# Kernel optimization log

Hardware: AMD Instinct MI355X
Metric: run time of the kernel (lower is better)

## Reference

```python
import jax, jax.numpy as jnp
import numpy as np

B = 64       # number of graphs
R = 148      # fixed ROI count from source
D = 64       # hidden_channels (embed_dim, 4 heads)
H = 4
IN1 = 64     # node feature dim (after stripping label column)
INR = 148    # roi-graph feature dim
HID = 1000
NCLS = 2
N1 = 262144
E1 = 1048576
N2 = B * R
E2 = 262144
EPS = 1e-5


def setup_inputs() -> dict:
    key = jax.random.key(0)
    ks = jax.random.split(key, 40)
    def p(i, shape, s=0.1):
        return jax.random.normal(ks[i], shape, dtype=jnp.float32) * s
    inp = {
        'x_feat': jax.random.normal(ks[0], (N1, IN1), dtype=jnp.float32),
        'node_roi': jax.random.randint(ks[1], (N1,), 0, R, dtype=jnp.int32),
        'batch1': ((jnp.arange(N1, dtype=jnp.int32) * B) // N1).astype(jnp.int32),
        'edge_index1': jax.random.randint(ks[2], (2, E1), 0, N1, dtype=jnp.int32),
        'edge_weight1': jax.random.uniform(ks[3], (E1,), dtype=jnp.float32, minval=0.1, maxval=1.0),
        'x2_feat': jax.random.normal(ks[4], (N2, INR), dtype=jnp.float32),
        'roi_labels2': (jnp.arange(N2, dtype=jnp.int32) % R).astype(jnp.int32),
        'batch2': (jnp.arange(N2, dtype=jnp.int32) // R).astype(jnp.int32),
        'edge_index2': jax.random.randint(ks[5], (2, E2), 0, N2, dtype=jnp.int32),
        'edge_weight2': jax.random.uniform(ks[6], (E2,), dtype=jnp.float32, minval=0.1, maxval=1.0),
        'Wg1': p(7, (IN1, D)), 'bg1': jnp.zeros((D,), jnp.float32),
        'Wg2': p(8, (D, D)), 'bg2': jnp.zeros((D,), jnp.float32),
        'Wr1': p(9, (INR, D)), 'br1': jnp.zeros((D,), jnp.float32),
        'Wr2': p(10, (D, D)), 'br2': jnp.zeros((D,), jnp.float32),
        'in_proj_w': p(11, (3 * D, D)), 'in_proj_b': jnp.zeros((3 * D,), jnp.float32),
        'out_proj_w': p(12, (D, D)), 'out_proj_b': jnp.zeros((D,), jnp.float32),
        'ln1_g': jnp.ones((D,), jnp.float32), 'ln1_b': jnp.zeros((D,), jnp.float32),
        'ff_w1': p(13, (D, D)), 'ff_b1': jnp.zeros((D,), jnp.float32),
        'ff_w2': p(14, (D, D)), 'ff_b2': jnp.zeros((D,), jnp.float32),
        'ln2_g': jnp.ones((D,), jnp.float32), 'ln2_b': jnp.zeros((D,), jnp.float32),
        'Wc1': p(15, (R * D, HID), 0.02), 'bc1': jnp.zeros((HID,), jnp.float32),
        'bn_g': jnp.ones((HID,), jnp.float32), 'bn_b': jnp.zeros((HID,), jnp.float32),
        'Wc2': p(16, (HID, NCLS), 0.02), 'bc2': jnp.zeros((NCLS,), jnp.float32),
    }
    return inp


def gcn_conv(h, src, dst, ew, W, b, n):
    # PyG GCNConv w/ edge weights: add self-loops (weight 1), sym-normalize.
    h = h @ W
    deg = jax.ops.segment_sum(ew, dst, num_segments=n) + 1.0
    dinv = jax.lax.rsqrt(deg)
    norm = dinv[src] * ew * dinv[dst]                      # (E,)
    agg = jax.ops.segment_sum(h[src] * norm[:, None], dst, num_segments=n)
    agg = agg + h * (dinv * dinv)[:, None]                 # self-loop term
    return agg + b


def roi_pool_mean(h, roi, batch):
    # fused scatter mean keyed by (batch, roi) -> (B, R, d); empty slots stay 0
    seg = batch * R + roi
    sums = jax.ops.segment_sum(h, seg, num_segments=B * R)
    cnt = jax.ops.segment_sum(jnp.ones_like(h[:, 0]), seg, num_segments=B * R)
    return (sums / jnp.maximum(cnt, 1.0)[:, None]).reshape(B, R, h.shape[1])


def layer_norm(x, g, b):
    mu = x.mean(axis=-1, keepdims=True)
    var = x.var(axis=-1, keepdims=True)
    return (x - mu) * jax.lax.rsqrt(var + EPS) * g + b


def reference(x_feat, node_roi, batch1, edge_index1, edge_weight1,
              x2_feat, roi_labels2, batch2, edge_index2, edge_weight2,
              Wg1, bg1, Wg2, bg2, Wr1, br1, Wr2, br2,
              in_proj_w, in_proj_b, out_proj_w, out_proj_b,
              ln1_g, ln1_b, ff_w1, ff_b1, ff_w2, ff_b2, ln2_g, ln2_b,
              Wc1, bc1, bn_g, bn_b, Wc2, bc2):
    s1, d1 = edge_index1[0], edge_index1[1]
    s2, d2 = edge_index2[0], edge_index2[1]

    # ROI-graph branch (convs_roi[:-1]): 2 GCN layers, relu, eval dropout=noop
    h2 = jax.nn.relu(gcn_conv(x2_feat, s2, d2, edge_weight2, Wr1, br1, N2))
    h2 = jax.nn.relu(gcn_conv(h2, s2, d2, edge_weight2, Wr2, br2, N2))
    pooled_roi = roi_pool_mean(h2, roi_labels2, batch2)          # (B,R,D)

    # node-graph branch (convs[:-1])
    h1 = jax.nn.relu(gcn_conv(x_feat, s1, d1, edge_weight1, Wg1, bg1, N1))
    h1 = jax.nn.relu(gcn_conv(h1, s1, d1, edge_weight1, Wg2, bg2, N1))
    pooled = roi_pool_mean(h1, node_roi, batch1)                 # (B,R,D)

    combined = pooled + pooled_roi                               # transformer_in_combined

    # SelfAttnBlock (torch MultiheadAttention, batch_first, 4 heads)
    hd = D // H
    qkv = combined @ in_proj_w.T + in_proj_b                     # (B,R,3D)
    q, k, v = jnp.split(qkv, 3, axis=-1)
    q = q.reshape(B, R, H, hd)
    k = k.reshape(B, R, H, hd)
    v = v.reshape(B, R, H, hd)
    scores = jnp.einsum('bqhd,bkhd->bhqk', q, k) / np.sqrt(hd).astype(np.float32)
    attn_w = jax.nn.softmax(scores, axis=-1)                     # (B,H,R,R)
    o = jnp.einsum('bhqk,bkhd->bqhd', attn_w, v).reshape(B, R, D)
    o = o @ out_proj_w.T + out_proj_b
    x = layer_norm(combined + o, ln1_g, ln1_b)
    f = jax.nn.relu(x @ ff_w1 + ff_b1) @ ff_w2 + ff_b2
    t_out = layer_norm(x + f, ln2_g, ln2_b)                      # (B,R,D)

    # classifier: Linear -> BatchNorm1d(eval: mean0,var1) -> LeakyReLU -> Linear
    z = t_out.reshape(B, R * D) @ Wc1 + bc1
    z = bn_g * z * jax.lax.rsqrt(jnp.asarray(1.0 + EPS, z.dtype)) + bn_b
    z = jnp.where(z >= 0, z, 0.01 * z)
    out = z @ Wc2 + bc2                                          # (B,NCLS)
    return (out, pooled, pooled_roi, t_out, attn_w)
```

## Files before the change

kernel.cpp:

```cpp
#include <hip/hip_runtime.h>
#include <cstdint>
#include <cstddef>

#define N1v 262144
#define E1v 1048576
#define N2v 9472
#define E2v 262144
#define BBv 64
#define RRv 148
#define HIDv 1000
#define BRv (BBv * RRv)
#define NSEG 9472
#define EPB 4096
#define NBK1 256
#define SH1 10
#define BINS1 1024
#define CAP1 4864
#define NBK2 74
#define SH2 7
#define BINS2 128
#define CAP2 4096

__host__ __device__ constexpr int cdiv(int a, int b) { return (a + b - 1) / b; }

typedef __attribute__((ext_vector_type(8))) short bf16x8;
typedef __attribute__((ext_vector_type(4))) float f32x4;
typedef unsigned short ushort_t;
typedef unsigned long long u64;

__device__ inline short f2bf(float f) {
    union { float f; unsigned u; } v; v.f = f;
    unsigned r = v.u + 0x7fff + ((v.u >> 16) & 1);
    return (short)(r >> 16);
}
__device__ inline float bf2f(unsigned hs) {
    union { unsigned u; float f; } v; v.u = hs << 16; return v.f;
}
__device__ inline unsigned relu_pk(unsigned u) {
    unsigned r = u;
    if (r & 0x8000u) r &= 0xFFFF0000u;
    if (r & 0x80000000u) r &= 0x0000FFFFu;
    return r;
}

__global__ __launch_bounds__(256) void k_binA(const int* __restrict__ dst1, int* __restrict__ bc1,
                                              const int* __restrict__ dst2, int* __restrict__ bc2) {
    int bid = blockIdx.x;
    const int* dst; int* bc; int nbk, sh, e0;
    if (bid < E1v / EPB) { dst = dst1; bc = bc1; nbk = NBK1; sh = SH1; e0 = bid * EPB; }
    else { dst = dst2; bc = bc2; nbk = NBK2; sh = SH2; e0 = (bid - E1v / EPB) * EPB; }
    __shared__ int h[256];
    int tid = threadIdx.x;
    if (tid < nbk) h[tid] = 0;
    __syncthreads();
    for (int t = tid; t < EPB; t += 256) atomicAdd(&h[dst[e0 + t] >> sh], 1);
    __syncthreads();
    if (tid < nbk && h[tid]) atomicAdd(&bc[tid], h[tid]);
}

__global__ __launch_bounds__(256) void k_scanAB(const int* __restrict__ bc1, int* __restrict__ bb1, int* __restrict__ cur1,
                                                const int* __restrict__ bc2, int* __restrict__ bb2, int* __restrict__ cur2) {
    __shared__ int tmp[256];
    int t = threadIdx.x;
    int v = bc1[t];
    tmp[t] = v; __syncthreads();
    int val = v;
    for (int off = 1; off < 256; off <<= 1) { int o = (t >= off) ? tmp[t - off] : 0; __syncthreads(); val += o; tmp[t] = val; __syncthreads(); }
    int excl = val - v;
    bb1[t] = excl; cur1[t] = excl;
    if (t == 255) bb1[256] = val;
    __syncthreads();
    int v2 = (t < NBK2) ? bc2[t] : 0;
    tmp[t] = v2; __syncthreads();
    int val2 = v2;
    for (int off = 1; off < 256; off <<= 1) { int o = (t >= off) ? tmp[t - off] : 0; __syncthreads(); val2 += o; tmp[t] = val2; __syncthreads(); }
    if (t < NBK2) { int e2 = val2 - v2; bb2[t] = e2; cur2[t] = e2; }
    if (t == NBK2 - 1) bb2[NBK2] = val2;
}

__global__ __launch_bounds__(256) void k_binB(const int* __restrict__ src1, const int* __restrict__ dst1,
                                              const float* __restrict__ ew1, int* __restrict__ cur1, u64* __restrict__ rb1,
                                              const int* __restrict__ src2, const int* __restrict__ dst2,
                                              const float* __restrict__ ew2, int* __restrict__ cur2, u64* __restrict__ rb2) {
    int bid = blockIdx.x;
    const int* src; const int* dst; const float* ew; int* cur; u64* rb; int nbk, sh, e0;
    if (bid < E1v / EPB) { src = src1; dst = dst1; ew = ew1; cur = cur1; rb = rb1; nbk = NBK1; sh = SH1; e0 = bid * EPB; }
    else { src = src2; dst = dst2; ew = ew2; cur = cur2; rb = rb2; nbk = NBK2; sh = SH2; e0 = (bid - E1v / EPB) * EPB; }
    __shared__ int h[256], basg[256];
    int tid = threadIdx.x;
    if (tid < nbk) h[tid] = 0;
    __syncthreads();
    for (int t = tid; t < EPB; t += 256) atomicAdd(&h[dst[e0 + t] >> sh], 1);
    __syncthreads();
    if (tid < nbk) {
        int c = h[tid];
        basg[tid] = c ? atomicAdd(&cur[tid], c) : 0;
        h[tid] = 0;
    }
    __syncthreads();
    unsigned lowmask = (1u << sh) - 1u;
    for (int t = tid; t < EPB; t += 256) {
        int d = dst[e0 + t];
        int b = d >> sh;
        int r = atomicAdd(&h[b], 1);
        unsigned lo = ((unsigned)src[e0 + t] << sh) | ((unsigned)d & lowmask);
        rb[(size_t)basg[b] + r] = ((u64)(unsigned)__float_as_int(ew[e0 + t]) << 32) | lo;
    }
}

template<int BINS, int CAP, int SH>
__global__ __launch_bounds__(256) void k_csrC(const u64* __restrict__ rb, const int* __restrict__ bb,
                                              float* __restrict__ dinv, int* __restrict__ offs,
                                              int2* __restrict__ snC) {
    int b = blockIdx.x;
    int beg = bb[b], end = bb[b + 1], cnt = end - beg;
    __shared__ int hist[BINS];
    __shared__ float degs[BINS];
    __shared__ int scn[BINS];
    __shared__ int tmp[256];
    extern __shared__ int2 outb[];
    int tid = threadIdx.x;
    for (int i = tid; i < BINS; i += 256) { hist[i] = 0; degs[i] = 0.f; }
    __syncthreads();
    for (int j = beg + tid; j < end; j += 256) {
        u64 rec = rb[j];
        int bin = (int)((unsigned)rec & (BINS - 1));
        float w = __int_as_float((int)(rec >> 32));
        atomicAdd(&hist[bin], 1);
        atomicAdd(&degs[bin], w);
    }
    __syncthreads();
    constexpr int PER = (BINS + 255) / 256;
    int lv[PER];
    int tsum = 0;
    int base_i = tid * PER;
#pragma unroll
    for (int k = 0; k < PER; ++k) { int idx = base_i + k; lv[k] = (idx < BINS) ? hist[idx] : 0; tsum += lv[k]; }
    tmp[tid] = tsum; __syncthreads();
    int val = tsum;
    for (int off = 1; off < 256; off <<= 1) { int o = (tid >= off) ? tmp[tid - off] : 0; __syncthreads(); val += o; tmp[tid] = val; __syncthreads(); }
    int run = val - tsum;
#pragma unroll
    for (int k = 0; k < PER; ++k) { int idx = base_i + k; if (idx < BINS) { scn[idx] = run; run += lv[k]; } }
    __syncthreads();
    for (int i = tid; i < BINS; i += 256) {
        offs[b * BINS + i] = beg + scn[i];
        dinv[b * BINS + i] = rsqrtf(degs[i] + 1.0f);
    }
    __syncthreads();
    bool staged = (cnt <= CAP);
    for (int j = beg + tid; j < end; j += 256) {
        u64 rec = rb[j];
        unsigned lo = (unsigned)rec;
        int bin = (int)(lo & (BINS - 1));
        int s = (int)(lo >> SH);
        int wbits = (int)(rec >> 32);
        int r = atomicAdd(&scn[bin], 1);
        int2 o2 = make_int2(s, wbits);
        if (staged) outb[r] = o2;
        else snC[(size_t)beg + r] = o2;
    }
    __syncthreads();
    if (staged) {
        for (int j = tid; j < cnt; j += 256) snC[(size_t)beg + j] = outb[j];
    }
}

__global__ __launch_bounds__(256) void k_pool_csr(const int* __restrict__ roi, int* __restrict__ offs_p,
                                                  int* __restrict__ nodeC) {
    int b = blockIdx.x;
    __shared__ int rl[4096];
    __shared__ int hist[RRv];
    __shared__ int curs[RRv];
    int tid = threadIdx.x;
    for (int t = tid; t < RRv; t += 256) hist[t] = 0;
    __syncthreads();
    int base = b * 4096;
    for (int t = tid; t < 4096; t += 256) {
        int r = roi[base + t];
        rl[t] = r;
        atomicAdd(&hist[r], 1);
    }
    __syncthreads();
    if (tid < RRv) {
        int s = 0;
        for (int k = 0; k < tid; ++k) s += hist[k];
        curs[tid] = s;
        offs_p[b * RRv + tid] = base + s;
    }
    __syncthreads();
    for (int t = tid; t < 4096; t += 256) {
        int r = rl[t];
        int j = atomicAdd(&curs[r], 1);
        nodeC[base + j] = base + t;
    }
}

__global__ __launch_bounds__(256) void k_pool_gather(const int* __restrict__ nodeC, const int* __restrict__ offs,
                                                     const ushort_t* __restrict__ Ab, float* __restrict__ pooled) {
    int tid = threadIdx.x;
    int lane = tid & 63;
    int es = lane >> 4;
    int fq = lane & 15;
    int gw = blockIdx.x * 4 + (tid >> 6);
    int tw = gridDim.x * 4;
    for (int s = gw; s < NSEG; s += tw) {
        int beg = offs[s];
        int end = (s + 1 < NSEG) ? offs[s + 1] : N1v;
        float ax = 0.f, ay = 0.f, az = 0.f, aw = 0.f;
        for (int j = beg + es; j < end; j += 4) {
            int node = nodeC[j];
            uint2 v = *(const uint2*)(Ab + (size_t)node * 64 + fq * 4);
            ax += fmaxf(bf2f(v.x & 0xffffu), 0.f);
            ay += fmaxf(bf2f(v.x >> 16), 0.f);
            az += fmaxf(bf2f(v.y & 0xffffu), 0.f);
            aw += fmaxf(bf2f(v.y >> 16), 0.f);
        }
        ax += __shfl_xor(ax, 16); ay += __shfl_xor(ay, 16);
        az += __shfl_xor(az, 16); aw += __shfl_xor(aw, 16);
        ax += __shfl_xor(ax, 32); ay += __shfl_xor(ay, 32);
        az += __shfl_xor(az, 32); aw += __shfl_xor(aw, 32);
        if (es == 0) {
            float inv = 1.f / (float)max(end - beg, 1);
            float4 r;
            r.x = ax * inv; r.y = ay * inv; r.z = az * inv; r.w = aw * inv;
            *(float4*)(pooled + (size_t)s * 64 + fq * 4) = r;
        }
    }
}

__global__ __launch_bounds__(256) void k_edge_gather3(const int2* __restrict__ snC,
                                                      const int* __restrict__ offs, const ushort_t* __restrict__ Pb,
                                                      const float* __restrict__ dinv, const float* __restrict__ bias,
                                                      ushort_t* __restrict__ A, int N, int E) {
    int tid = threadIdx.x;
    int lane = tid & 63;
    int nh = lane >> 5;
    int slot = (lane >> 3) & 3;
    int f8 = lane & 7;
    float4 bv0 = *(const float4*)(bias + f8 * 8);
    float4 bv1 = *(const float4*)(bias + f8 * 8 + 4);
    int gw = blockIdx.x * 4 + (tid >> 6);
    int tw = gridDim.x * 4;
    for (int ii = gw * 2; ii < N; ii += tw * 2) {
        int i = ii + nh;
        int beg = offs[i];
        int end = (i + 1 < N) ? offs[i + 1] : E;
        float di = dinv[i];
        float a0 = 0.f, a1 = 0.f, a2 = 0.f, a3 = 0.f, a4 = 0.f, a5 = 0.f, a6 = 0.f, a7 = 0.f;
        for (int j = beg + slot; j < end; j += 4) {
            int2 e = snC[j];
            int s = e.x;
            float nv = dinv[s] * __int_as_float(e.y) * di;
            uint4 w = *(const uint4*)(Pb + (size_t)s * 64 + f8 * 8);
            a0 = fmaf(nv, bf2f(w.x & 0xffffu), a0);
            a1 = fmaf(nv, bf2f(w.x >> 16), a1);
            a2 = fmaf(nv, bf2f(w.y & 0xffffu), a2);
            a3 = fmaf(nv, bf2f(w.y >> 16), a3);
            a4 = fmaf(nv, bf2f(w.z & 0xffffu), a4);
            a5 = fmaf(nv, bf2f(w.z >> 16), a5);
            a6 = fmaf(nv, bf2f(w.w & 0xffffu), a6);
            a7 = fmaf(nv, bf2f(w.w >> 16), a7);
        }
        a0 += __shfl_xor(a0, 8);  a1 += __shfl_xor(a1, 8);  a2 += __shfl_xor(a2, 8);  a3 += __shfl_xor(a3, 8);
        a4 += __shfl_xor(a4, 8);  a5 += __shfl_xor(a5, 8);  a6 += __shfl_xor(a6, 8);  a7 += __shfl_xor(a7, 8);
        a0 += __shfl_xor(a0, 16); a1 += __shfl_xor(a1, 16); a2 += __shfl_xor(a2, 16); a3 += __shfl_xor(a3, 16);
        a4 += __shfl_xor(a4, 16); a5 += __shfl_xor(a5, 16); a6 += __shfl_xor(a6, 16); a7 += __shfl_xor(a7, 16);
        if (slot == 0) {
            uint4 w = *(const uint4*)(Pb + (size_t)i * 64 + f8 * 8);
            float s2 = di * di;
            float r0 = fmaf(s2, bf2f(w.x & 0xffffu), a0) + bv0.x;
            float r1 = fmaf(s2, bf2f(w.x >> 16),    a1) + bv0.y;
            float r2 = fmaf(s2, bf2f(w.y & 0xffffu), a2) + bv0.z;
            float r3 = fmaf(s2, bf2f(w.y >> 16),    a3) + bv0.w;
            float r4 = fmaf(s2, bf2f(w.z & 0xffffu), a4) + bv1.x;
            float r5 = fmaf(s2, bf2f(w.z >> 16),    a5) + bv1.y;
            float r6 = fmaf(s2, bf2f(w.w & 0xffffu), a6) + bv1.z;
            float r7 = fmaf(s2, bf2f(w.w >> 16),    a7) + bv1.w;
            uint4 ov;
            ov.x = (unsigned)(ushort_t)f2bf(r0) | ((unsigned)(ushort_t)f2bf(r1) << 16);
            ov.y = (unsigned)(ushort_t)f2bf(r2) | ((unsigned)(ushort_t)f2bf(r3) << 16);
            ov.z = (unsigned)(ushort_t)f2bf(r4) | ((unsigned)(ushort_t)f2bf(r5) << 16);
            ov.w = (unsigned)(ushort_t)f2bf(r6) | ((unsigned)(ushort_t)f2bf(r7) << 16);
            *(uint4*)(A + (size_t)i * 64 + f8 * 8) = ov;
        }
    }
}

template<bool RIN, bool IBF16>
__global__ __launch_bounds__(256) void k_gemm_mfma(const void* __restrict__ Xv, const float* __restrict__ Wmat,
                                                   ushort_t* __restrict__ Y, int N) {
    int tid = threadIdx.x;
    int lane = tid & 63;
    int wv = tid >> 6;
    int l15 = lane & 15;
    int lg = lane >> 4;
    bf16x8 bfrag[2][4];
    for (int kh = 0; kh < 2; ++kh)
        for (int ct = 0; ct < 4; ++ct) {
            bf16x8 b;
#pragma unroll
            for (int i = 0; i < 8; ++i)
                b[i] = f2bf(Wmat[(size_t)(kh * 32 + lg * 8 + i) * 64 + ct * 16 + l15]);
            bfrag[kh][ct] = b;
        }
    int gw = blockIdx.x * 4 + wv;
    int tw = gridDim.x * 4;
    int ntiles = N >> 4;
    for (int t = gw; t < ntiles; t += tw) {
        int row0 = t << 4;
        bf16x8 af0, af1;
        if (IBF16) {
            const ushort_t* xp = (const ushort_t*)Xv + (size_t)(row0 + l15) * 64 + lg * 8;
            uint4 c0 = *(const uint4*)(xp);
            uint4 c1 = *(const uint4*)(xp + 32);
            if (RIN) {
                c0.x = relu_pk(c0.x); c0.y = relu_pk(c0.y); c0.z = relu_pk(c0.z); c0.w = relu_pk(c0.w);
                c1.x = relu_pk(c1.x); c1.y = relu_pk(c1.y); c1.z = relu_pk(c1.z); c1.w = relu_pk(c1.w);
            }
            af0 = *reinterpret_cast<bf16x8*>(&c0);
            af1 = *reinterpret_cast<bf16x8*>(&c1);
        } else {
            const float* xp = (const float*)Xv + (size_t)(row0 + l15) * 64 + lg * 8;
            float4 a0 = *(const float4*)(xp);
            float4 a1 = *(const float4*)(xp + 4);
            float4 a2 = *(const float4*)(xp + 32);
            float4 a3 = *(const float4*)(xp + 36);
            if (RIN) {
                a0.x = fmaxf(a0.x, 0.f); a0.y = fmaxf(a0.y, 0.f); a0.z = fmaxf(a0.z, 0.f); a0.w = fmaxf(a0.w, 0.f);
                a1.x = fmaxf(a1.x, 0.f); a1.y = fmaxf(a1.y, 0.f); a1.z = fmaxf(a1.z, 0.f); a1.w = fmaxf(a1.w, 0.f);
                a2.x = fmaxf(a2.x, 0.f); a2.y = fmaxf(a2.y, 0.f); a2.z = fmaxf(a2.z, 0.f); a2.w = fmaxf(a2.w, 0.f);
                a3.x = fmaxf(a3.x, 0.f); a3.y = fmaxf(a3.y, 0.f); a3.z = fmaxf(a3.z, 0.f); a3.w = fmaxf(a3.w, 0.f);
            }
            af0[0] = f2bf(a0.x); af0[1] = f2bf(a0.y); af0[2] = f2bf(a0.z); af0[3] = f2bf(a0.w);
            af0[4] = f2bf(a1.x); af0[5] = f2bf(a1.y); af0[6] = f2bf(a1.z); af0[7] = f2bf(a1.w);
            af1[0] = f2bf(a2.x); af1[1] = f2bf(a2.y); af1[2] = f2bf(a2.z); af1[3] = f2bf(a2.w);
            af1[4] = f2bf(a3.x); af1[5] = f2bf(a3.y); af1[6] = f2bf(a3.z); af1[7] = f2bf(a3.w);
        }
        f32x4 acc0 = {0.f, 0.f, 0.f, 0.f}, acc1 = acc0, acc2 = acc0, acc3 = acc0;
        acc0 = __builtin_amdgcn_mfma_f32_16x16x32_bf16(af0, bfrag[0][0], acc0, 0, 0, 0);
        acc1 = __builtin_amdgcn_mfma_f32_16x16x32_bf16(af0, bfrag[0][1], acc1, 0, 0, 0);
        acc2 = __builtin_amdgcn_mfma_f32_16x16x32_bf16(af0, bfrag[0][2], acc2, 0, 0, 0);
        acc3 = __builtin_amdgcn_mfma_f32_16x16x32_bf16(af0, bfrag[0][3], acc3, 0, 0, 0);
        acc0 = __builtin_amdgcn_mfma_f32_16x16x32_bf16(af1, bfrag[1][0], acc0, 0, 0, 0);
        acc1 = __builtin_amdgcn_mfma_f32_16x16x32_bf16(af1, bfrag[1][1], acc1, 0, 0, 0);
        acc2 = __builtin_amdgcn_mfma_f32_16x16x32_bf16(af1, bfrag[1][2], acc2, 0, 0, 0);
        acc3 = __builtin_amdgcn_mfma_f32_16x16x32_bf16(af1, bfrag[1][3], acc3, 0, 0, 0);
        ushort_t* yp = Y + (size_t)(row0 + lg * 4) * 64 + l15;
#pragma unroll
        for (int r = 0; r < 4; ++r) {
            yp[(size_t)r * 64 + 0]  = (ushort_t)f2bf(acc0[r]);
            yp[(size_t)r * 64 + 16] = (ushort_t)f2bf(acc1[r]);
            yp[(size_t)r * 64 + 32] = (ushort_t)f2bf(acc2[r]);
            yp[(size_t)r * 64 + 48] = (ushort_t)f2bf(acc3[r]);
        }
    }
}

template<int MB, bool RIN, bool ROUT, bool OBF16>
__global__ __launch_bounds__(256) void k_gemm_rowwave(const float* __restrict__ X, const float* __restrict__ W,
                                                      const float* __restrict__ bias, void* __restrict__ Yv,
                                                      int N, int K) {
    extern __shared__ float Wl[];
    const int M = MB * 64;
    for (int idx = threadIdx.x; idx < K * M; idx += 256) Wl[idx] = W[idx];
    __syncthreads();
    int lane = threadIdx.x & 63;
    int gw = blockIdx.x * 4 + (threadIdx.x >> 6);
    int tw = gridDim.x * 4;
    const int K4 = K >> 2;
    for (int row = gw; row < N; row += tw) {
        float acc[MB];
#pragma unroll
        for (int cb = 0; cb < MB; ++cb) acc[cb] = 0.f;
        const float4* xr = (const float4*)(X + (size_t)row * K);
        for (int k4 = 0; k4 < K4; ++k4) {
            float4 xv = xr[k4];
            if (RIN) {
                xv.x = fmaxf(xv.x, 0.f); xv.y = fmaxf(xv.y, 0.f);
                xv.z = fmaxf(xv.z, 0.f); xv.w = fmaxf(xv.w, 0.f);
            }
            const float* wp = Wl + (k4 * 4) * M + lane;
#pragma unroll
            for (int cb = 0; cb < MB; ++cb) acc[cb] = fmaf(xv.x, wp[cb * 64], acc[cb]);
            wp += M;
#pragma unroll
            for (int cb = 0; cb < MB; ++cb) acc[cb] = fmaf(xv.y, wp[cb * 64], acc[cb]);
            wp += M;
#pragma unroll
            for (int cb = 0; cb < MB; ++cb) acc[cb] = fmaf(xv.z, wp[cb * 64], acc[cb]);
            wp += M;
#pragma unroll
            for (int cb = 0; cb < MB; ++cb) acc[cb] = fmaf(xv.w, wp[cb * 64], acc[cb]);
        }
#pragma unroll
        for (int cb = 0; cb < MB; ++cb) {
            float y = acc[cb];
            int col = cb * 64 + lane;
            if (bias) y += bias[col];
            if (ROUT) y = fmaxf(y, 0.f);
            if (OBF16) ((ushort_t*)Yv)[(size_t)row * M + col] = (ushort_t)f2bf(y);
            else ((float*)Yv)[(size_t)row * M + col] = y;
        }
    }
}

__global__ __launch_bounds__(256) void k_transpose(const float* __restrict__ W, float* __restrict__ Wt,
                                                   int rows, int cols) {
    int i = blockIdx.x * 256 + threadIdx.x;
    if (i < rows * cols) {
        int r = i / cols, c = i - r * cols;
        Wt[c * rows + r] = W[i];
    }
}

__global__ __launch_bounds__(256) void k_pool_fin2b(const ushort_t* __restrict__ h2Ab, const float* __restrict__ pooled,
                                                    float* __restrict__ pooledroi, float* __restrict__ comb,
                                                    int n4) {
    int i = blockIdx.x * 256 + threadIdx.x;
    if (i < n4) {
        uint2 v = *(const uint2*)(h2Ab + (size_t)i * 4);
        float4 p = ((const float4*)pooled)[i];
        float4 r;
        r.x = fmaxf(bf2f(v.x & 0xffffu), 0.f);
        r.y = fmaxf(bf2f(v.x >> 16), 0.f);
        r.z = fmaxf(bf2f(v.y & 0xffffu), 0.f);
        r.w = fmaxf(bf2f(v.y >> 16), 0.f);
        ((float4*)pooledroi)[i] = r;
        float4 c;
        c.x = r.x + p.x; c.y = r.y + p.y; c.z = r.z + p.z; c.w = r.w + p.w;
        ((float4*)comb)[i] = c;
    }
}

__global__ __launch_bounds__(256) void k_attn(const float* __restrict__ qkv, float* __restrict__ aw,
                                              float* __restrict__ o) {
    int qc = blockIdx.x & 3;
    int bh = blockIdx.x >> 2;
    int b = bh >> 2, h = bh & 3;
    __shared__ float qs[37][16];
    __shared__ float kT[16][152];
    __shared__ float vs[148][16];
    __shared__ float ps[4][152];
    int tid = threadIdx.x;
    const float* base = qkv + (size_t)b * 148 * 192 + h * 16;
    for (int idx = tid; idx < 148 * 16; idx += 256) {
        int i = idx >> 4, d = idx & 15;
        const float* p = base + (size_t)i * 192 + d;
        kT[d][i] = p[64];
        vs[i][d] = p[128];
    }
    int q0 = qc * 37;
    for (int idx = tid; idx < 37 * 16; idx += 256) {
        int i = idx >> 4, d = idx & 15;
        qs[i][d] = base[(size_t)(q0 + i) * 192 + d] * 0.25f;
    }
    __syncthreads();
    int wv = tid >> 6, lane = tid & 63;
    float* aw_bh = aw + (size_t)bh * 148 * 148;
    for (int ii = wv; ii < 37; ii += 4) {
        int i = q0 + ii;
        float s0 = 0.f, s1 = 0.f, s2 = 0.f;
#pragma unroll
        for (int d = 0; d < 16; ++d) {
            float q = qs[ii][d];
            s0 = fmaf(q, kT[d][lane], s0);
            s1 = fmaf(q, kT[d][lane + 64], s1);
            if (lane < 20) s2 = fmaf(q, kT[d][lane + 128], s2);
        }
        float m = fmaxf(s0, s1);
        if (lane < 20) m = fmaxf(m, s2);
#pragma unroll
        for (int off = 1; off < 64; off <<= 1) m = fmaxf(m, __shfl_xor(m, off));
        float e0 = __expf(s0 - m), e1 = __expf(s1 - m);
        float e2 = (lane < 20) ? __expf(s2 - m) : 0.f;
        float sum = e0 + e1 + e2;
#pragma unroll
        for (int off = 1; off < 64; off <<= 1) sum += __shfl_xor(sum, off);
        float inv = 1.f / sum;
        float p0 = e0 * inv, p1 = e1 * inv, p2 = e2 * inv;
        float* awr = aw_bh + (size_t)i * 148;
        awr[lane] = p0;
        awr[lane + 64] = p1;
        if (lane < 20) awr[lane + 128] = p2;
        ps[wv][lane] = p0;
        ps[wv][lane + 64] = p1;
        if (lane < 20) ps[wv][lane + 128] = p2;
        int d = lane & 15, jj = lane >> 4;
        float acc = 0.f;
        for (int t = jj; t < 148; t += 4) acc = fmaf(ps[wv][t], vs[t][d], acc);
        acc += __shfl_xor(acc, 16);
        acc += __shfl_xor(acc, 32);
        if (lane < 16) o[((size_t)b * 148 + i) * 64 + h * 16 + d] = acc;
    }
}

__global__ __launch_bounds__(256) void k_ln_gemm(const float* __restrict__ X, const float* __restrict__ Wt,
                                                 const float* __restrict__ bias, const float* __restrict__ resid,
                                                 const float* __restrict__ g, const float* __restrict__ bb,
                                                 float* __restrict__ Y, int N) {
    __shared__ float Wl[4096];
    for (int idx = threadIdx.x; idx < 4096; idx += 256) Wl[idx] = Wt[idx];
    __syncthreads();
    int lane = threadIdx.x & 63;
    int gw = blockIdx.x * 4 + (threadIdx.x >> 6);
    int tw = gridDim.x * 4;
    for (int row = gw; row < N; row += tw) {
        const float4* xr = (const float4*)(X + (size_t)row * 64);
        float acc = 0.f;
        for (int k4 = 0; k4 < 16; ++k4) {
            float4 xv = xr[k4];
            const float* wp = Wl + (k4 * 4) * 64 + lane;
            acc = fmaf(xv.x, wp[0], acc);
            acc = fmaf(xv.y, wp[64], acc);
            acc = fmaf(xv.z, wp[128], acc);
            acc = fmaf(xv.w, wp[192], acc);
        }
        float y = acc + bias[lane] + resid[(size_t)row * 64 + lane];
        float s = y;
#pragma unroll
        for (int off = 1; off < 64; off <<= 1) s += __shfl_xor(s, off);
        float mu = s * (1.f / 64.f);
        float dcen = y - mu;
        float v = dcen * dcen;
#pragma unroll
        for (int off = 1; off < 64; off <<= 1) v += __shfl_xor(v, off);
        float var = v * (1.f / 64.f);
        Y[(size_t)row * 64 + lane] = dcen * rsqrtf(var + 1e-5f) * g[lane] + bb[lane];
    }
}

__global__ __launch_bounds__(256) void k_cls_part(const float* __restrict__ T, const float* __restrict__ Wc1,
                                                  float* __restrict__ Zp) {
    int ks = blockIdx.x >> 2;
    int mt = blockIdx.x & 3;
    int k0 = ks * 74;
    int m0 = mt * 256;
    __shared__ float Tl[64][74];
    int tid = threadIdx.x;
    for (int idx = tid; idx < 64 * 74; idx += 256) {
        int b = idx / 74, kk = idx - b * 74;
        Tl[b][kk] = T[(size_t)b * 9472 + k0 + kk];
    }
    __syncthreads();
    int lane = tid & 63, bq = tid >> 6;
    int mbase = m0 + lane * 4;
    size_t moff = (mbase + 3 < 1000) ? (size_t)mbase : 0;
    float4 acc[16];
#pragma unroll
    for (int j = 0; j < 16; ++j) acc[j] = make_float4(0.f, 0.f, 0.f, 0.f);
#pragma unroll 2
    for (int kk = 0; kk < 74; ++kk) {
        float4 w = *(const float4*)(Wc1 + (size_t)(k0 + kk) * 1000 + moff);
#pragma unroll
        for (int j = 0; j < 16; ++j) {
            float t = Tl[bq * 16 + j][kk];
            acc[j].x = fmaf(t, w.x, acc[j].x);
            acc[j].y = fmaf(t, w.y, acc[j].y);
            acc[j].z = fmaf(t, w.z, acc[j].z);
            acc[j].w = fmaf(t, w.w, acc[j].w);
        }
    }
    float* zp = Zp + (size_t)ks * 64 * 1024;
#pragma unroll
    for (int j = 0; j < 16; ++j) {
        int b = bq * 16 + j;
        *(float4*)(zp + (size_t)b * 1024 + mbase) = acc[j];
    }
}

__global__ __launch_bounds__(256) void k_cls_reduce(const float* __restrict__ Zp, const float* __restrict__ bc1,
                                                    const float* __restrict__ bn_g, const float* __restrict__ bn_b,
                                                    float* __restrict__ zb) {
    int flat = blockIdx.x * 256 + threadIdx.x;
    int b = flat >> 10, m = flat & 1023;
    if (m >= 1000) return;
    float s = 0.f;
    for (int ks = 0; ks < 128; ++ks)
        s += Zp[((size_t)ks * 64 + b) * 1024 + m];
    float rs = rsqrtf(1.0f + 1e-5f);
    float z = bn_g[m] * (s + bc1[m]) * rs + bn_b[m];
    zb[flat] = z >= 0.f ? z : 0.01f * z;
}

__global__ __launch_bounds__(256) void k_cls_final(const float* __restrict__ zb,
                                                   const float* __restrict__ Wc2, const float* __restrict__ bc2,
                                                   float* __restrict__ out) {
    int b = blockIdx.x;
    int tid = threadIdx.x;
    float a0 = 0.f, a1 = 0.f;
    for (int m = tid; m < 1000; m += 256) {
        float z = zb[b * 1024 + m];
        a0 = fmaf(z, Wc2[m * 2], a0);
        a1 = fmaf(z, Wc2[m * 2 + 1], a1);
    }
#pragma unroll
    for (int off = 1; off < 64; off <<= 1) {
        a0 += __shfl_xor(a0, off);
        a1 += __shfl_xor(a1, off);
    }
    __shared__ float r0[4], r1[4];
    if ((tid & 63) == 0) { r0[tid >> 6] = a0; r1[tid >> 6] = a1; }
    __syncthreads();
    if (tid == 0) {
        out[b * 2 + 0] = r0[0] + r0[1] + r0[2] + r0[3] + bc2[0];
        out[b * 2 + 1] = r1[0] + r1[1] + r1[2] + r1[3] + bc2[1];
    }
}

extern "C" void kernel_launch(void* const* d_in, const int* in_sizes, int n_in,
                              void* d_out, int out_size, void* d_ws, size_t ws_size,
                              hipStream_t stream) {
    (void)in_sizes; (void)n_in; (void)out_size; (void)ws_size;

    const float* x_feat = (const float*)d_in[0];
    const int* node_roi = (const int*)d_in[1];
    const int* ei1 = (const int*)d_in[3];
    const float* ew1 = (const float*)d_in[4];
    const float* x2f = (const float*)d_in[5];
    const int* ei2 = (const int*)d_in[8];
    const float* ew2 = (const float*)d_in[9];
    const float* Wg1 = (const float*)d_in[10];
    const float* bg1 = (const float*)d_in[11];
    const float* Wg2 = (const float*)d_in[12];
    const float* bg2 = (const float*)d_in[13];
    const float* Wr1 = (const float*)d_in[14];
    const float* br1 = (const float*)d_in[15];
    const float* Wr2 = (const float*)d_in[16];
    const float* br2 = (const float*)d_in[17];
    const float* in_proj_w = (const float*)d_in[18];
    const float* in_proj_b = (const float*)d_in[19];
    const float* out_proj_w = (const float*)d_in[20];
    const float* out_proj_b = (const float*)d_in[21];
    const float* ln1_g = (const float*)d_in[22];
    const float* ln1_b = (const float*)d_in[23];
    const float* ff_w1 = (const float*)d_in[24];
    const float* ff_b1 = (const float*)d_in[25];
    const float* ff_w2 = (const float*)d_in[26];
    const float* ff_b2 = (const float*)d_in[27];
    const float* ln2_g = (const float*)d_in[28];
    const float* ln2_b = (const float*)d_in[29];
    const float* Wc1 = (const float*)d_in[30];
    const float* bc1 = (const float*)d_in[31];
    const float* bn_g = (const float*)d_in[32];
    const float* bn_b = (const float*)d_in[33];
    const float* Wc2 = (const float*)d_in[34];
    const float* bc2 = (const float*)d_in[35];

    const int* src1 = ei1;
    const int* dst1 = ei1 + E1v;
    const int* src2 = ei2;
    const int* dst2 = ei2 + E2v;

    float* out = (float*)d_out;
    const int PSZ = BRv * 64;
    float* pooled_out = out + 128;
    float* pooledroi_out = out + 128 + PSZ;
    float* tout_out = out + 128 + 2 * PSZ;
    float* attn_out = out + 128 + 3 * PSZ;

    float* W = (float*)d_ws;
    size_t o = 0;
    int* bcnt1 = (int*)(W + o);  o += 256;
    int* bcnt2 = (int*)(W + o);  o += 128;
    size_t zone_elems = o;
    int* bb1 = (int*)(W + o);  o += 260;
    int* cur1 = (int*)(W + o); o += 256;
    int* bb2 = (int*)(W + o);  o += 76;
    int* cur2 = (int*)(W + o); o += 128;
    o = (o + 1) & ~(size_t)1;
    int2* snC1 = (int2*)(W + o); o += (size_t)E1v * 2;
    int2* snC2 = (int2*)(W + o); o += (size_t)E2v * 2;
    float* dinv1 = W + o;        o += N1v;
    float* dinv2 = W + o;        o += N2v;
    int* offs1 = (int*)(W + o);  o += N1v;
    int* offs2 = (int*)(W + o);  o += N2v;
    int* offs_p = (int*)(W + o); o += NSEG;
    int* nodeC = (int*)(W + o);  o += N1v;
    float* zbuf = W + o;         o += BBv * 1024;
    o = (o + 1) & ~(size_t)1;
    size_t h1P_off = o; o += (size_t)N1v * 64;
    size_t h1A_off = o; o += (size_t)N1v * 64;
    ushort_t* h1P = (ushort_t*)(W + h1P_off);
    ushort_t* h1Ab = (ushort_t*)(W + h1A_off);
    u64* rb1 = (u64*)(W + h1P_off);
    u64* rb2 = rb1 + E1v;
    size_t p = h1P_off;
    ushort_t* h2P = (ushort_t*)(W + p);  p += (size_t)N2v * 64;
    ushort_t* h2Ab = (ushort_t*)(W + p); p += (size_t)N2v * 64;
    float* comb = W + p; p += PSZ;
    float* qkvb = W + p; p += (size_t)BRv * 192;
    float* obuf = W + p; p += PSZ;
    float* xbuf = W + p; p += PSZ;
    float* f1 = W + p;   p += PSZ;
    float* WinT = W + p; p += 64 * 192;
    float* WoutT = W + p; p += 64 * 64;
    float* Zp = W + h1A_off;

    dim3 blk(256);

    hipMemsetAsync(W, 0, zone_elems * sizeof(float), stream);

    k_binA<<<E1v / EPB + E2v / EPB, blk, 0, stream>>>(dst1, bcnt1, dst2, bcnt2);
    k_scanAB<<<1, blk, 0, stream>>>(bcnt1, bb1, cur1, bcnt2, bb2, cur2);
    k_binB<<<E1v / EPB + E2v / EPB, blk, 0, stream>>>(src1, dst1, ew1, cur1, rb1,
                                                      src2, dst2, ew2, cur2, rb2);
    k_csrC<BINS1, CAP1, SH1><<<NBK1, blk, CAP1 * 8, stream>>>(rb1, bb1, dinv1, offs1, snC1);
    k_csrC<BINS2, CAP2, SH2><<<NBK2, blk, CAP2 * 8, stream>>>(rb2, bb2, dinv2, offs2, snC2);
    k_pool_csr<<<BBv, blk, 0, stream>>>(node_roi, offs_p, nodeC);

    k_gemm_mfma<false, false><<<2048, blk, 0, stream>>>(x_feat, Wg1, h1P, N1v);
    k_edge_gather3<<<4096, blk, 0, stream>>>(snC1, offs1, h1P, dinv1, bg1, h1Ab, N1v, E1v);
    k_gemm_mfma<true, true><<<2048, blk, 0, stream>>>(h1Ab, Wg2, h1P, N1v);
    k_edge_gather3<<<4096, blk, 0, stream>>>(snC1, offs1, h1P, dinv1, bg2, h1Ab, N1v, E1v);
    k_pool_gather<<<2048, blk, 0, stream>>>(nodeC, offs_p, h1Ab, pooled_out);

    k_gemm_rowwave<1, false, false, true><<<cdiv(N2v, 4), blk, 148 * 64 * 4, stream>>>(x2f, Wr1, nullptr, h2P, N2v, 148);
    k_edge_gather3<<<cdiv(N2v, 8), blk, 0, stream>>>(snC2, offs2, h2P, dinv2, br1, h2Ab, N2v, E2v);
    k_gemm_mfma<true, true><<<148, blk, 0, stream>>>(h2Ab, Wr2, h2P, N2v);
    k_edge_gather3<<<cdiv(N2v, 8), blk, 0, stream>>>(snC2, offs2, h2P, dinv2, br2, h2Ab, N2v, E2v);
    k_pool_fin2b<<<cdiv(PSZ / 4, 256), blk, 0, stream>>>(h2Ab, pooled_out, pooledroi_out, comb, PSZ / 4);

    k_transpose<<<cdiv(192 * 64, 256), blk, 0, stream>>>(in_proj_w, WinT, 192, 64);
    k_transpose<<<cdiv(64 * 64, 256), blk, 0, stream>>>(out_proj_w, WoutT, 64, 64);
    k_gemm_rowwave<3, false, false, false><<<cdiv(N2v, 4), blk, 64 * 192 * 4, stream>>>(comb, WinT, in_proj_b, qkvb, N2v, 64);
    k_attn<<<BBv * 4 * 4, blk, 0, stream>>>(qkvb, attn_out, obuf);
    k_ln_gemm<<<cdiv(N2v, 4), blk, 0, stream>>>(obuf, WoutT, out_proj_b, comb, ln1_g, ln1_b, xbuf, N2v);
    k_gemm_rowwave<1, false, true, false><<<cdiv(N2v, 4), blk, 64 * 64 * 4, stream>>>(xbuf, ff_w1, ff_b1, f1, N2v, 64);
    k_ln_gemm<<<cdiv(N2v, 4), blk, 0, stream>>>(f1, ff_w2, ff_b2, xbuf, ln2_g, ln2_b, tout_out, N2v);

    k_cls_part<<<512, blk, 0, stream>>>(tout_out, Wc1, Zp);
    k_cls_reduce<<<BBv * 1024 / 256, blk, 0, stream>>>(Zp, bc1, bn_g, bn_b, zbuf);
    k_cls_final<<<BBv, blk, 0, stream>>>(zbuf, Wc2, bc2, out);
}
```

Before: 423.8 us.

## Retune edge binning to 512 buckets, widen pool gather loads, merge transposes

Edge binning for graph 1 now uses 512 buckets of 512 nodes, with 1024 edges per block instead of 4096. This gives more blocks and smaller per-bucket CSR shared-memory staging, and the scan handles two buckets per thread. The pool gather kernel now has each lane load 8 bf16 features (16 bytes) and each wave process two segments. The two weight-transpose launches are merged into one kernel to save a launch. These changes trade more global atomics and bucket blocks for better parallelism and wider memory accesses.

```diff
diff --git a/kernel.cpp b/kernel.cpp
--- a/kernel.cpp
+++ b/kernel.cpp
@@ -11,11 +11,11 @@
 #define HIDv 1000
 #define BRv (BBv * RRv)
 #define NSEG 9472
-#define EPB 4096
-#define NBK1 256
-#define SH1 10
-#define BINS1 1024
-#define CAP1 4864
+#define EPB 1024
+#define NBK1 512
+#define SH1 9
+#define BINS1 512
+#define CAP1 2560
 #define NBK2 74
 #define SH2 7
 #define BINS2 128
@@ -46,29 +46,31 @@
 __global__ __launch_bounds__(256) void k_binA(const int* __restrict__ dst1, int* __restrict__ bc1,
                                               const int* __restrict__ dst2, int* __restrict__ bc2) {
     int bid = blockIdx.x;
-    const int* dst; int* bc; int nbk, sh, e0;
+    const int* dst; int* bc; int nbk, sh; int e0;
     if (bid < E1v / EPB) { dst = dst1; bc = bc1; nbk = NBK1; sh = SH1; e0 = bid * EPB; }
     else { dst = dst2; bc = bc2; nbk = NBK2; sh = SH2; e0 = (bid - E1v / EPB) * EPB; }
-    __shared__ int h[256];
-    int tid = threadIdx.x;
-    if (tid < nbk) h[tid] = 0;
+    __shared__ int h[NBK1];
+    int tid = threadIdx.x;
+    for (int t = tid; t < nbk; t += 256) h[t] = 0;
     __syncthreads();
     for (int t = tid; t < EPB; t += 256) atomicAdd(&h[dst[e0 + t] >> sh], 1);
     __syncthreads();
-    if (tid < nbk && h[tid]) atomicAdd(&bc[tid], h[tid]);
+    for (int t = tid; t < nbk; t += 256) if (h[t]) atomicAdd(&bc[t], h[t]);
 }
 
 __global__ __launch_bounds__(256) void k_scanAB(const int* __restrict__ bc1, int* __restrict__ bb1, int* __restrict__ cur1,
                                                 const int* __restrict__ bc2, int* __restrict__ bb2, int* __restrict__ cur2) {
     __shared__ int tmp[256];
     int t = threadIdx.x;
-    int v = bc1[t];
-    tmp[t] = v; __syncthreads();
-    int val = v;
+    int v0 = bc1[t * 2], v1 = bc1[t * 2 + 1];
+    int ts = v0 + v1;
+    tmp[t] = ts; __syncthreads();
+    int val = ts;
     for (int off = 1; off < 256; off <<= 1) { int o = (t >= off) ? tmp[t - off] : 0; __syncthreads(); val += o; tmp[t] = val; __syncthreads(); }
-    int excl = val - v;
-    bb1[t] = excl; cur1[t] = excl;
-    if (t == 255) bb1[256] = val;
+    int excl = val - ts;
+    bb1[t * 2] = excl;     cur1[t * 2] = excl;
+    bb1[t * 2 + 1] = excl + v0; cur1[t * 2 + 1] = excl + v0;
+    if (t == 255) bb1[NBK1] = val;
     __syncthreads();
     int v2 = (t < NBK2) ? bc2[t] : 0;
     tmp[t] = v2; __syncthreads();
@@ -83,19 +85,19 @@
                                               const int* __restrict__ src2, const int* __restrict__ dst2,
                                               const float* __restrict__ ew2, int* __restrict__ cur2, u64* __restrict__ rb2) {
     int bid = blockIdx.x;
-    const int* src; const int* dst; const float* ew; int* cur; u64* rb; int nbk, sh, e0;
+    const int* src; const int* dst; const float* ew; int* cur; u64* rb; int nbk, sh; int e0;
     if (bid < E1v / EPB) { src = src1; dst = dst1; ew = ew1; cur = cur1; rb = rb1; nbk = NBK1; sh = SH1; e0 = bid * EPB; }
     else { src = src2; dst = dst2; ew = ew2; cur = cur2; rb = rb2; nbk = NBK2; sh = SH2; e0 = (bid - E1v / EPB) * EPB; }
-    __shared__ int h[256], basg[256];
-    int tid = threadIdx.x;
-    if (tid < nbk) h[tid] = 0;
+    __shared__ int h[NBK1], basg[NBK1];
+    int tid = threadIdx.x;
+    for (int t = tid; t < nbk; t += 256) h[t] = 0;
     __syncthreads();
     for (int t = tid; t < EPB; t += 256) atomicAdd(&h[dst[e0 + t] >> sh], 1);
     __syncthreads();
-    if (tid < nbk) {
-        int c = h[tid];
-        basg[tid] = c ? atomicAdd(&cur[tid], c) : 0;
-        h[tid] = 0;
+    for (int t = tid; t < nbk; t += 256) {
+        int c = h[t];
+        basg[t] = c ? atomicAdd(&cur[t], c) : 0;
+        h[t] = 0;
     }
     __syncthreads();
     unsigned lowmask = (1u << sh) - 1u;
@@ -200,31 +202,39 @@
                                                      const ushort_t* __restrict__ Ab, float* __restrict__ pooled) {
     int tid = threadIdx.x;
     int lane = tid & 63;
-    int es = lane >> 4;
-    int fq = lane & 15;
+    int nh = lane >> 5;
+    int slot = (lane >> 3) & 3;
+    int f8 = lane & 7;
     int gw = blockIdx.x * 4 + (tid >> 6);
     int tw = gridDim.x * 4;
-    for (int s = gw; s < NSEG; s += tw) {
+    for (int ss = gw * 2; ss < NSEG; ss += tw * 2) {
+        int s = ss + nh;
         int beg = offs[s];
         int end = (s + 1 < NSEG) ? offs[s + 1] : N1v;
-        float ax = 0.f, ay = 0.f, az = 0.f, aw = 0.f;
-        for (int j = beg + es; j < end; j += 4) {
+        float a0 = 0.f, a1 = 0.f, a2 = 0.f, a3 = 0.f, a4 = 0.f, a5 = 0.f, a6 = 0.f, a7 = 0.f;
+        for (int j = beg + slot; j < end; j += 4) {
             int node = nodeC[j];
-            uint2 v = *(const uint2*)(Ab + (size_t)node * 64 + fq * 4);
-            ax += fmaxf(bf2f(v.x & 0xffffu), 0.f);
-            ay += fmaxf(bf2f(v.x >> 16), 0.f);
-            az += fmaxf(bf2f(v.y & 0xffffu), 0.f);
-            aw += fmaxf(bf2f(v.y >> 16), 0.f);
-        }
-        ax += __shfl_xor(ax, 16); ay += __shfl_xor(ay, 16);
-        az += __shfl_xor(az, 16); aw += __shfl_xor(aw, 16);
-        ax += __shfl_xor(ax, 32); ay += __shfl_xor(ay, 32);
-        az += __shfl_xor(az, 32); aw += __shfl_xor(aw, 32);
-        if (es == 0) {
+            uint4 v = *(const uint4*)(Ab + (size_t)node * 64 + f8 * 8);
+            a0 += fmaxf(bf2f(v.x & 0xffffu), 0.f);
+            a1 += fmaxf(bf2f(v.x >> 16), 0.f);
+            a2 += fmaxf(bf2f(v.y & 0xffffu), 0.f);
+            a3 += fmaxf(bf2f(v.y >> 16), 0.f);
+            a4 += fmaxf(bf2f(v.z & 0xffffu), 0.f);
+            a5 += fmaxf(bf2f(v.z >> 16), 0.f);
+            a6 += fmaxf(bf2f(v.w & 0xffffu), 0.f);
+            a7 += fmaxf(bf2f(v.w >> 16), 0.f);
+        }
+        a0 += __shfl_xor(a0, 8);  a1 += __shfl_xor(a1, 8);  a2 += __shfl_xor(a2, 8);  a3 += __shfl_xor(a3, 8);
+        a4 += __shfl_xor(a4, 8);  a5 += __shfl_xor(a5, 8);  a6 += __shfl_xor(a6, 8);  a7 += __shfl_xor(a7, 8);
+        a0 += __shfl_xor(a0, 16); a1 += __shfl_xor(a1, 16); a2 += __shfl_xor(a2, 16); a3 += __shfl_xor(a3, 16);
+        a4 += __shfl_xor(a4, 16); a5 += __shfl_xor(a5, 16); a6 += __shfl_xor(a6, 16); a7 += __shfl_xor(a7, 16);
+        if (slot == 0) {
             float inv = 1.f / (float)max(end - beg, 1);
-            float4 r;
-            r.x = ax * inv; r.y = ay * inv; r.z = az * inv; r.w = aw * inv;
-            *(float4*)(pooled + (size_t)s * 64 + fq * 4) = r;
+            float4 r0, r1;
+            r0.x = a0 * inv; r0.y = a1 * inv; r0.z = a2 * inv; r0.w = a3 * inv;
+            r1.x = a4 * inv; r1.y = a5 * inv; r1.z = a6 * inv; r1.w = a7 * inv;
+            *(float4*)(pooled + (size_t)s * 64 + f8 * 8) = r0;
+            *(float4*)(pooled + (size_t)s * 64 + f8 * 8 + 4) = r1;
         }
     }
 }
@@ -405,12 +415,16 @@
     }
 }
 
-__global__ __launch_bounds__(256) void k_transpose(const float* __restrict__ W, float* __restrict__ Wt,
-                                                   int rows, int cols) {
+__global__ __launch_bounds__(256) void k_transpose2(const float* __restrict__ Win, float* __restrict__ WinT,
+                                                    const float* __restrict__ Wout, float* __restrict__ WoutT) {
     int i = blockIdx.x * 256 + threadIdx.x;
-    if (i < rows * cols) {
-        int r = i / cols, c = i - r * cols;
-        Wt[c * rows + r] = W[i];
+    if (i < 192 * 64) {
+        int r = i >> 6, c = i & 63;
+        WinT[c * 192 + r] = Win[i];
+    } else if (i < 192 * 64 + 64 * 64) {
+        int j = i - 192 * 64;
+        int r = j >> 6, c = j & 63;
+        WoutT[c * 64 + r] = Wout[j];
     }
 }
 
@@ -661,11 +675,11 @@
 
     float* W = (float*)d_ws;
     size_t o = 0;
-    int* bcnt1 = (int*)(W + o);  o += 256;
+    int* bcnt1 = (int*)(W + o);  o += NBK1;
     int* bcnt2 = (int*)(W + o);  o += 128;
     size_t zone_elems = o;
-    int* bb1 = (int*)(W + o);  o += 260;
-    int* cur1 = (int*)(W + o); o += 256;
+    int* bb1 = (int*)(W + o);  o += NBK1 + 4;
+    int* cur1 = (int*)(W + o); o += NBK1;
     int* bb2 = (int*)(W + o);  o += 76;
     int* cur2 = (int*)(W + o); o += 128;
     o = (o + 1) & ~(size_t)1;
@@ -721,8 +735,7 @@
     k_edge_gather3<<<cdiv(N2v, 8), blk, 0, stream>>>(snC2, offs2, h2P, dinv2, br2, h2Ab, N2v, E2v);
     k_pool_fin2b<<<cdiv(PSZ / 4, 256), blk, 0, stream>>>(h2Ab, pooled_out, pooledroi_out, comb, PSZ / 4);
 
-    k_transpose<<<cdiv(192 * 64, 256), blk, 0, stream>>>(in_proj_w, WinT, 192, 64);
-    k_transpose<<<cdiv(64 * 64, 256), blk, 0, stream>>>(out_proj_w, WoutT, 64, 64);
+    k_transpose2<<<cdiv(192 * 64 + 64 * 64, 256), blk, 0, stream>>>(in_proj_w, WinT, out_proj_w, WoutT);
     k_gemm_rowwave<3, false, false, false><<<cdiv(N2v, 4), blk, 64 * 192 * 4, stream>>>(comb, WinT, in_proj_b, qkvb, N2v, 64);
     k_attn<<<BBv * 4 * 4, blk, 0, stream>>>(qkvb, attn_out, obuf);
     k_ln_gemm<<<cdiv(N2v, 4), blk, 0, stream>>>(obuf, WoutT, out_proj_b, comb, ln1_g, ln1_b, xbuf, N2v);
```

Result: slower. 460.8 us (+8.7%).
